# Kernel tuning notes

Hardware: AMD Instinct MI355X
Metric: run time of the kernel (lower is better)

Reference implementation:

```python
import jax, jax.numpy as jnp
import numpy as np

NATOMS = 50000          # edge_vector rows
M = 3 * NATOMS          # attention nodes = numel(edge_vector)
NE = 1500000            # edges
NH, DH = 4, 16          # num_heads, head dim (out_dim // num_heads)


def _glorot(key, shape):
    fan_in, fan_out = shape
    lim = (6.0 / (fan_in + fan_out)) ** 0.5
    return jax.random.uniform(key, shape, jnp.float32, -lim, lim)


def setup_inputs() -> dict:
    key = jax.random.key(0)
    ks = jax.random.split(key, 12)
    inp = {
        "node_attr": jax.random.normal(ks[0], (2, M), jnp.float32),
        "edge_index": jax.random.randint(ks[1], (2, NE), 0, M, jnp.int64),
        "edge_feature": jax.random.normal(ks[2], (NE, 4), jnp.float32),
        "edge_vector": jax.random.normal(ks[3], (NATOMS, 3), jnp.float32),
        # parameters (hardcoded layer sizes in the torch module)
        "W1": _glorot(ks[4], (1, 4)),   "b1": jnp.zeros((4,), jnp.float32),
        "W2": _glorot(ks[5], (4, 16)),  "b2": jnp.zeros((16,), jnp.float32),
        "W": _glorot(ks[6], (16, 64)),  "b": jnp.zeros((64,), jnp.float32),
        "Wout": _glorot(ks[7], (64, 16)), "bout": jnp.zeros((16,), jnp.float32),
        "Wout1": _glorot(ks[8], (16, 1)), "bout1": jnp.zeros((1,), jnp.float32),
    }
    return inp


def reference(node_attr, edge_index, edge_feature, edge_vector,
              W1, b1, W2, b2, W, b, Wout, bout, Wout1, bout1):
    # node pathway: each scalar of edge_vector is one attention node
    h = edge_vector.reshape(-1, 1)                      # [M, 1]
    h = jax.nn.elu(h @ W1 + b1)                         # [M, 4]  (dropout = identity, eval)
    h = (h @ W2 + b2).reshape(-1, DH)                   # [M, 16]
    qkv = (h @ W + b).reshape(-1, NH, DH)               # [M, 4, 16]; Q==K==V (shared linear)

    # edge pathway
    e = jax.nn.elu(edge_feature @ W2 + b2)              # [Ne, 16]
    E = (e @ W + b).reshape(-1, NH, DH)                 # [Ne, 4, 16]

    src_idx = edge_index[0]
    dst_idx = edge_index[1]
    src = qkv[src_idx]                                  # K_h gather [Ne,4,16]
    dst = qkv[dst_idx]                                  # Q_h gather [Ne,4,16]
    score = (src * dst) * (1.0 / np.sqrt(DH)) * E       # edge-conditioned scores
    score = jnp.exp(jnp.clip(score.sum(-1, keepdims=True), -5.0, 5.0))  # [Ne,4,1]

    msg = qkv[src_idx] * score                          # V_h gather * score
    wV = jax.ops.segment_sum(msg, dst_idx, num_segments=M)      # [M,4,16]
    Z = jax.ops.segment_sum(score, dst_idx, num_segments=M)     # [M,4,1]

    h_out = (wV / (Z + 1e-6)).reshape(-1, NH * DH)      # [M, 64]
    h_out = jax.nn.elu(h_out @ Wout + bout)             # [M, 16]
    h_out = (h_out @ Wout1 + bout1).reshape(-1, 3)      # [M/3, 3]
    return h_out
```

## Files before the change

kernel.cpp:

```cpp
#include <hip/hip_runtime.h>
#include <hip/hip_bf16.h>
#include <cstdint>

#define DEVI __device__ __forceinline__

typedef __attribute__((ext_vector_type(8))) short bf16x8;
typedef __attribute__((ext_vector_type(4))) float f32x4;

DEVI float bf2f(unsigned short u) {
    union { unsigned int i; float f; } v; v.i = ((unsigned int)u) << 16; return v.f;
}
DEVI float ldf(const void* p, long long i, int f32) {
    return f32 ? ((const float*)p)[i] : bf2f(((const unsigned short*)p)[i]);
}
DEVI unsigned short f2bfu(float x) {
    __hip_bfloat16 h = __float2bfloat16(x);
    return *reinterpret_cast<unsigned short*>(&h);
}
DEVI short f2bf(float x) { return (short)f2bfu(x); }
DEVI float eluf(float x) { return x > 0.f ? x : __expf(x) - 1.f; }

__global__ __launch_bounds__(64) void detect_k(
    const int* __restrict__ eidx32, const unsigned int* __restrict__ wbits,
    int* __restrict__ flags)
{
    int t = threadIdx.x;
    int odd = eidx32[2 * t + 1];
    unsigned long long bz = __ballot(odd == 0);
    unsigned int w = wbits[t];
    unsigned int ex = (w >> 23) & 0xFF;
    unsigned long long bf = __ballot(ex >= 100 && ex <= 130);
    if (t == 0) {
        flags[0] = (bz == ~0ULL) ? 1 : 0;
        flags[1] = (__popcll(bf) >= 48) ? 1 : 0;
    }
}

__global__ __launch_bounds__(256) void node_qkv_k(
    const int* __restrict__ flags,
    const void* __restrict__ evec,
    const void* __restrict__ W1, const void* __restrict__ b1,
    const void* __restrict__ W2, const void* __restrict__ b2,
    const void* __restrict__ W,  const void* __restrict__ b,
    unsigned short* __restrict__ qkvb, int M_)
{
    __shared__ float sW[1024], sW2[64], sb[64], sb2[16], sW1[4], sb1[4];
    int t = threadIdx.x;
    int f32 = flags[1];
    for (int i = t; i < 1024; i += 256) sW[i] = ldf(W, i, f32);
    if (t < 64) { sW2[t] = ldf(W2, t, f32); sb[t] = ldf(b, t, f32); }
    if (t < 16) sb2[t] = ldf(b2, t, f32);
    if (t < 4)  { sW1[t] = ldf(W1, t, f32); sb1[t] = ldf(b1, t, f32); }
    __syncthreads();

    int m = blockIdx.x * 256 + t;
    if (m >= M_) return;

    float x = ldf(evec, m, f32);
    float h1[4];
    #pragma unroll
    for (int j = 0; j < 4; ++j) h1[j] = eluf(fmaf(x, sW1[j], sb1[j]));
    float h2[16];
    #pragma unroll
    for (int k = 0; k < 16; ++k) h2[k] = sb2[k];
    #pragma unroll
    for (int j = 0; j < 4; ++j)
        #pragma unroll
        for (int k = 0; k < 16; ++k) h2[k] = fmaf(h1[j], sW2[j*16 + k], h2[k]);

    uint4* op = (uint4*)(qkvb + (size_t)m * 64);
    for (int g = 0; g < 8; ++g) {
        float v[8];
        #pragma unroll
        for (int j = 0; j < 8; ++j) {
            int c = g * 8 + j;
            float a = sb[c];
            #pragma unroll
            for (int k = 0; k < 16; ++k) a = fmaf(h2[k], sW[k*64 + c], a);
            v[j] = a;
        }
        uint4 pk;
        pk.x = (unsigned)f2bfu(v[0]) | ((unsigned)f2bfu(v[1]) << 16);
        pk.y = (unsigned)f2bfu(v[2]) | ((unsigned)f2bfu(v[3]) << 16);
        pk.z = (unsigned)f2bfu(v[4]) | ((unsigned)f2bfu(v[5]) << 16);
        pk.w = (unsigned)f2bfu(v[6]) | ((unsigned)f2bfu(v[7]) << 16);
        op[g] = pk;
    }
}

__global__ __launch_bounds__(256) void hist_k(
    const int* __restrict__ flags, const int* __restrict__ eidx32,
    int* __restrict__ counts, int* __restrict__ rank, int NE_)
{
    int e0 = (blockIdx.x * 256 + threadIdx.x) * 4;
    if (e0 >= NE_) return;
    int i64 = flags[0];
    if (e0 + 3 < NE_) {
        int d[4];
        if (i64) {
            long long w = 2LL * (NE_ + (long long)e0);
            int4 a = *(const int4*)(eidx32 + w);
            int4 b = *(const int4*)(eidx32 + w + 4);
            d[0] = a.x; d[1] = a.z; d[2] = b.x; d[3] = b.z;
        } else {
            #pragma unroll
            for (int i = 0; i < 4; ++i) d[i] = eidx32[(long long)NE_ + e0 + i];
        }
        int r[4];
        #pragma unroll
        for (int i = 0; i < 4; ++i) r[i] = atomicAdd(&counts[d[i]], 1);
        *(int4*)(rank + e0) = make_int4(r[0], r[1], r[2], r[3]);
    } else {
        for (int e = e0; e < NE_; ++e) {
            int dst = i64 ? eidx32[2LL * (NE_ + (long long)e)]
                          : eidx32[(long long)NE_ + e];
            rank[e] = atomicAdd(&counts[dst], 1);
        }
    }
}

__global__ __launch_bounds__(256) void scan_a_k(
    const int* __restrict__ counts, int* __restrict__ bsum, int M_)
{
    __shared__ int s[256];
    int t = threadIdx.x;
    int g4 = blockIdx.x * 256 + t;
    int i0 = g4 * 4;
    int v = 0;
    if (i0 + 3 < M_) {
        int4 c = ((const int4*)counts)[g4];
        v = c.x + c.y + c.z + c.w;
    } else {
        for (int k = 0; k < 4 && i0 + k < M_; ++k) v += counts[i0 + k];
    }
    s[t] = v; __syncthreads();
    for (int off = 128; off > 0; off >>= 1) {
        if (t < off) s[t] += s[t + off];
        __syncthreads();
    }
    if (t == 0) bsum[blockIdx.x] = s[0];
}

__global__ __launch_bounds__(256) void scan_b_k(
    const int* __restrict__ bsum, int* __restrict__ bexcl, int nb,
    int* __restrict__ offsets, int M_, int NE_)
{
    __shared__ int s[256];
    int t = threadIdx.x;
    int mine = (t < nb) ? bsum[t] : 0;
    s[t] = mine; __syncthreads();
    for (int off = 1; off < 256; off <<= 1) {
        int v = (t >= off) ? s[t - off] : 0;
        __syncthreads();
        s[t] += v;
        __syncthreads();
    }
    if (t < nb) bexcl[t] = s[t] - mine;
    if (t == 0) offsets[M_] = NE_;
}

__global__ __launch_bounds__(256) void scan_c_k(
    const int* __restrict__ counts, const int* __restrict__ bexcl,
    int* __restrict__ offsets, int M_)
{
    __shared__ int s[256];
    int t = threadIdx.x;
    int g4 = blockIdx.x * 256 + t;
    int i0 = g4 * 4;
    int c0 = 0, c1 = 0, c2 = 0, c3 = 0;
    if (i0 + 3 < M_) {
        int4 c = ((const int4*)counts)[g4];
        c0 = c.x; c1 = c.y; c2 = c.z; c3 = c.w;
    } else {
        if (i0 + 0 < M_) c0 = counts[i0 + 0];
        if (i0 + 1 < M_) c1 = counts[i0 + 1];
        if (i0 + 2 < M_) c2 = counts[i0 + 2];
        if (i0 + 3 < M_) c3 = counts[i0 + 3];
    }
    int tsum = c0 + c1 + c2 + c3;
    s[t] = tsum; __syncthreads();
    for (int off = 1; off < 256; off <<= 1) {
        int v = (t >= off) ? s[t - off] : 0;
        __syncthreads();
        s[t] += v;
        __syncthreads();
    }
    int run = bexcl[blockIdx.x] + s[t] - tsum;
    if (i0 + 0 < M_) { offsets[i0+0] = run; run += c0; }
    if (i0 + 1 < M_) { offsets[i0+1] = run; run += c1; }
    if (i0 + 2 < M_) { offsets[i0+2] = run; run += c2; }
    if (i0 + 3 < M_) { offsets[i0+3] = run; run += c3; }
}

__global__ __launch_bounds__(256) void scatter_k(
    const int* __restrict__ flags, const int* __restrict__ eidx32,
    const void* __restrict__ efeat,
    const int* __restrict__ offsets, const int* __restrict__ rank,
    int4* __restrict__ sorted, int NE_)
{
    int e = blockIdx.x * 256 + threadIdx.x;
    if (e >= NE_) return;
    int i64 = flags[0];
    int f32 = flags[1];
    int src, dst;
    if (i64) { src = eidx32[2LL * e]; dst = eidx32[2LL * (NE_ + (long long)e)]; }
    else     { src = eidx32[e];       dst = eidx32[(long long)NE_ + e]; }

    unsigned int ef01, ef23;
    if (f32) {
        const float4 f = ((const float4*)efeat)[e];
        ef01 = (unsigned)f2bfu(f.x) | ((unsigned)f2bfu(f.y) << 16);
        ef23 = (unsigned)f2bfu(f.z) | ((unsigned)f2bfu(f.w) << 16);
    } else {
        const uint2 u = ((const uint2*)efeat)[e];
        ef01 = u.x; ef23 = u.y;
    }

    int pos = offsets[dst] + rank[e];
    sorted[pos] = make_int4(src, dst, (int)ef01, (int)ef23);
}

__global__ __launch_bounds__(256) void score_k(
    const int* __restrict__ flags, const int4* __restrict__ sorted,
    const void* __restrict__ W2, const void* __restrict__ b2,
    const void* __restrict__ W,  const void* __restrict__ b,
    const unsigned short* __restrict__ qkvb, float* __restrict__ score, int NE_)
{
    __shared__ float sW2[64], sb2[16];
    __shared__ float sE[4][16 * 68];
    int t = threadIdx.x;
    int f32 = flags[1];
    if (t < 64) sW2[t] = ldf(W2, t, f32);
    if (t < 16) sb2[t] = ldf(b2, t, f32);
    __syncthreads();

    int wv   = t >> 6;
    int lane = t & 63;
    int col  = lane & 15;
    int quad = lane >> 4;
    float* myE = &sE[wv][0];

    bf16x8 bfrag[4];
    float  bb[4];
    #pragma unroll
    for (int h = 0; h < 4; ++h) {
        #pragma unroll
        for (int jj = 0; jj < 8; ++jj) {
            int k = quad * 8 + jj;
            float wv_ = (k < 16) ? ldf(W, k * 64 + h * 16 + col, f32) : 0.f;
            bfrag[h][jj] = f2bf(wv_);
        }
        bb[h] = ldf(b, h * 16 + col, f32);
    }

    int j2 = lane >> 2, h2 = lane & 3;

    long long tiles = ((long long)NE_ + 15) >> 4;
    long long wid   = (long long)blockIdx.x * 4 + wv;
    long long nw    = (long long)gridDim.x * 4;

    long long tile = wid;
    int4 rec = make_int4(0, 0, 0, 0);
    if (tile < tiles) {
        int jA = (int)(tile << 4) + col;
        if (jA < NE_) rec = sorted[jA];
    }

    while (tile < tiles) {
        long long tnext = tile + nw;
        int4 recn = make_int4(0, 0, 0, 0);
        if (tnext < tiles) {
            int jB = (int)(tnext << 4) + col;
            if (jB < NE_) recn = sorted[jB];
        }

        int base = (int)(tile << 4);
        float ef0 = bf2f((unsigned short)((unsigned)rec.z & 0xffff));
        float ef1 = bf2f((unsigned short)((unsigned)rec.z >> 16));
        float ef2 = bf2f((unsigned short)((unsigned)rec.w & 0xffff));
        float ef3 = bf2f((unsigned short)((unsigned)rec.w >> 16));

        bf16x8 afrag;
        #pragma unroll
        for (int jj = 0; jj < 8; ++jj) {
            int k = quad * 8 + jj;
            float v = 0.f;
            if (k < 16) {
                v = eluf(fmaf(ef0, sW2[k],
                        fmaf(ef1, sW2[16 + k],
                        fmaf(ef2, sW2[32 + k],
                        fmaf(ef3, sW2[48 + k], sb2[k])))));
            }
            afrag[jj] = f2bf(v);
        }

        f32x4 acc[4];
        #pragma unroll
        for (int h = 0; h < 4; ++h) {
            acc[h] = (f32x4){0.f, 0.f, 0.f, 0.f};
            acc[h] = __builtin_amdgcn_mfma_f32_16x16x32_bf16(afrag, bfrag[h], acc[h], 0, 0, 0);
        }

        #pragma unroll
        for (int h = 0; h < 4; ++h)
            #pragma unroll
            for (int r = 0; r < 4; ++r)
                myE[(quad * 4 + r) * 68 + h * 16 + col] = acc[h][r] + bb[h];

        asm volatile("s_waitcnt lgkmcnt(0)" ::: "memory");

        int srcj = __shfl(rec.x, j2, 64);
        int dstj = __shfl(rec.y, j2, 64);

        const uint4* sp = (const uint4*)(qkvb + (size_t)srcj * 64 + h2 * 16);
        const uint4* dp = (const uint4*)(qkvb + (size_t)dstj * 64 + h2 * 16);
        uint4 sA = sp[0], sB = sp[1], dA = dp[0], dB = dp[1];

        const float4* ep = (const float4*)(myE + j2 * 68 + h2 * 16);
        float4 e0 = ep[0], e1 = ep[1], e2 = ep[2], e3 = ep[3];
        float E[16] = {e0.x,e0.y,e0.z,e0.w, e1.x,e1.y,e1.z,e1.w,
                       e2.x,e2.y,e2.z,e2.w, e3.x,e3.y,e3.z,e3.w};

        unsigned int su[8] = {sA.x,sA.y,sA.z,sA.w, sB.x,sB.y,sB.z,sB.w};
        unsigned int du[8] = {dA.x,dA.y,dA.z,dA.w, dB.x,dB.y,dB.z,dB.w};

        float sc = 0.f;
        #pragma unroll
        for (int i = 0; i < 8; ++i) {
            float s0 = bf2f((unsigned short)(su[i] & 0xffff));
            float s1 = bf2f((unsigned short)(su[i] >> 16));
            float d0 = bf2f((unsigned short)(du[i] & 0xffff));
            float d1 = bf2f((unsigned short)(du[i] >> 16));
            sc = fmaf(s0 * d0, E[2*i],   sc);
            sc = fmaf(s1 * d1, E[2*i+1], sc);
        }
        sc *= 0.25f;
        sc = fminf(fmaxf(sc, -5.f), 5.f);
        float s = __expf(sc);

        int jW = base + j2;
        if (jW < NE_) score[(size_t)jW * 4 + h2] = s;

        rec = recn;
        tile = tnext;
    }
}

__global__ __launch_bounds__(256) void accum_out_k(
    const int* __restrict__ flags,
    const int* __restrict__ offsets, const int4* __restrict__ sorted,
    const float* __restrict__ score, const unsigned short* __restrict__ qkvb,
    const void* __restrict__ Wout, const void* __restrict__ bout,
    const void* __restrict__ Wout1, const void* __restrict__ bout1,
    void* __restrict__ out, int M_)
{
    __shared__ float sWo[1024], sbo[16], sWo1[16];
    __shared__ float sbo1;
    int t = threadIdx.x;
    int f32 = flags[1];
    for (int i = t; i < 1024; i += 256) sWo[i] = ldf(Wout, i, f32);
    if (t < 16) { sbo[t] = ldf(bout, t, f32); sWo1[t] = ldf(Wout1, t, f32); }
    if (t == 0) sbo1 = ldf(bout1, 0, f32);
    __syncthreads();

    int gid = blockIdx.x * 256 + t;
    int m = gid >> 2;
    if (m >= M_) return;
    int h  = gid & 3;
    int hb = h * 16;

    int beg = offsets[m], end = offsets[m + 1];

    float acc[16];
    #pragma unroll
    for (int d = 0; d < 16; ++d) acc[d] = 0.f;
    float z = 0.f;

    int j = beg;
    for (; j + 4 <= end; j += 4) {
        int s4[4];
        float sc4[4];
        #pragma unroll
        for (int u = 0; u < 4; ++u) {
            s4[u]  = sorted[j + u].x;
            sc4[u] = score[(size_t)(j + u) * 4 + h];
        }
        uint4 qa[4], qb[4];
        #pragma unroll
        for (int u = 0; u < 4; ++u) {
            const uint4* p = (const uint4*)(qkvb + (size_t)s4[u] * 64 + hb);
            qa[u] = p[0]; qb[u] = p[1];
        }
        #pragma unroll
        for (int u = 0; u < 4; ++u) {
            float s = sc4[u];
            z += s;
            unsigned int q[8] = {qa[u].x,qa[u].y,qa[u].z,qa[u].w,
                                 qb[u].x,qb[u].y,qb[u].z,qb[u].w};
            #pragma unroll
            for (int i = 0; i < 8; ++i) {
                acc[2*i]   = fmaf(bf2f((unsigned short)(q[i] & 0xffff)), s, acc[2*i]);
                acc[2*i+1] = fmaf(bf2f((unsigned short)(q[i] >> 16)),    s, acc[2*i+1]);
            }
        }
    }
    for (; j < end; ++j) {
        int s0 = sorted[j].x;
        float sc0 = score[(size_t)j * 4 + h];
        const uint4* p0 = (const uint4*)(qkvb + (size_t)s0 * 64 + hb);
        uint4 a0 = p0[0], a1 = p0[1];
        z += sc0;
        unsigned int q0[8] = {a0.x,a0.y,a0.z,a0.w, a1.x,a1.y,a1.z,a1.w};
        #pragma unroll
        for (int i = 0; i < 8; ++i) {
            acc[2*i]   = fmaf(bf2f((unsigned short)(q0[i] & 0xffff)), sc0, acc[2*i]);
            acc[2*i+1] = fmaf(bf2f((unsigned short)(q0[i] >> 16)),    sc0, acc[2*i+1]);
        }
    }

    float zinv = 1.f / (z + 1e-6f);

    float p[16];
    #pragma unroll
    for (int jj = 0; jj < 16; ++jj) p[jj] = 0.f;
    #pragma unroll
    for (int d = 0; d < 16; ++d) {
        float hv = acc[d] * zinv;
        #pragma unroll
        for (int jj = 0; jj < 16; ++jj) p[jj] = fmaf(hv, sWo[(hb + d) * 16 + jj], p[jj]);
    }
    #pragma unroll
    for (int jj = 0; jj < 16; ++jj) {
        p[jj] += __shfl_xor(p[jj], 1, 64);
        p[jj] += __shfl_xor(p[jj], 2, 64);
    }
    if (h == 0) {
        float o = sbo1;
        #pragma unroll
        for (int jj = 0; jj < 16; ++jj) o = fmaf(eluf(p[jj] + sbo[jj]), sWo1[jj], o);
        if (f32) ((float*)out)[m] = o;
        else     ((__hip_bfloat16*)out)[m] = __float2bfloat16(o);
    }
}

extern "C" void kernel_launch(void* const* d_in, const int* in_sizes, int n_in,
                              void* d_out, int out_size, void* d_ws, size_t ws_size,
                              hipStream_t stream)
{
    const int*  eidx  = (const int*)d_in[1];
    const void* efeat = d_in[2];
    const void* evec  = d_in[3];
    const void* W1 = d_in[4],  *b1 = d_in[5];
    const void* W2 = d_in[6],  *b2 = d_in[7];
    const void* W  = d_in[8],  *b  = d_in[9];
    const void* Wout = d_in[10], *bout = d_in[11];
    const void* Wout1 = d_in[12], *bout1 = d_in[13];

    const int M_  = in_sizes[3];
    const int NE_ = in_sizes[1] / 2;
    const int nb  = (M_ + 1023) / 1024;

    char* wp = (char*)d_ws;
    int*            flags   = (int*)wp;                 wp += 16;
    unsigned short* qkvb    = (unsigned short*)wp;      wp += (size_t)M_ * 64 * 2;
    int*            counts  = (int*)wp;                 wp += (size_t)M_ * 4;
    int*            bsum    = (int*)wp;                 wp += 2048 * 4;
    int*            bexcl   = (int*)wp;                 wp += 2048 * 4;
    int*            offsets = (int*)wp;                 wp += ((size_t)M_ + 4) * 4;
    int*            rank    = (int*)wp;                 wp += (size_t)NE_ * 4;
    wp = (char*)(((uintptr_t)wp + 15) & ~(uintptr_t)15);
    int4*           sorted  = (int4*)wp;                wp += (size_t)NE_ * 16;
    float*          scoreB  = (float*)wp;

    detect_k<<<1, 64, 0, stream>>>(eidx, (const unsigned int*)W, flags);
    (void)hipMemsetAsync(counts, 0, (size_t)M_ * 4, stream);

    node_qkv_k<<<(M_ + 255) / 256, 256, 0, stream>>>(
        flags, evec, W1, b1, W2, b2, W, b, qkvb, M_);

    int q4 = (NE_ + 3) / 4;
    hist_k<<<(q4 + 255) / 256, 256, 0, stream>>>(flags, eidx, counts, rank, NE_);
    scan_a_k<<<nb, 256, 0, stream>>>(counts, bsum, M_);
    scan_b_k<<<1, 256, 0, stream>>>(bsum, bexcl, nb, offsets, M_, NE_);
    scan_c_k<<<nb, 256, 0, stream>>>(counts, bexcl, offsets, M_);
    scatter_k<<<(NE_ + 255) / 256, 256, 0, stream>>>(
        flags, eidx, efeat, offsets, rank, sorted, NE_);

    long long tiles = ((long long)NE_ + 15) / 16;
    int sblocks = (int)((tiles + 3) / 4);
    if (sblocks > 12288) sblocks = 12288;
    score_k<<<sblocks, 256, 0, stream>>>(
        flags, sorted, W2, b2, W, b, qkvb, scoreB, NE_);

    long long tot = (long long)M_ * 4;
    accum_out_k<<<(int)((tot + 255) / 256), 256, 0, stream>>>(
        flags, offsets, sorted, scoreB, qkvb,
        Wout, bout, Wout1, bout1, d_out, M_);
}
```

Before: 369.0 us.

## Partition score tiles per XCD and split accumulation across 8 lanes per node

Result: no change. 367.8 us (-0.3%).

```diff
diff --git a/kernel.cpp b/kernel.cpp
--- a/kernel.cpp
+++ b/kernel.cpp
@@ -256,20 +256,23 @@
     int j2 = lane >> 2, h2 = lane & 3;
 
     long long tiles = ((long long)NE_ + 15) >> 4;
-    long long wid   = (long long)blockIdx.x * 4 + wv;
-    long long nw    = (long long)gridDim.x * 4;
-
-    long long tile = wid;
+    long long Tr   = (tiles + 7) >> 3;
+    int       xcd  = blockIdx.x & 7;
+    int       lb   = blockIdx.x >> 3;
+    long long tEnd = (long long)(xcd + 1) * Tr; if (tEnd > tiles) tEnd = tiles;
+    long long stride = (long long)(gridDim.x >> 3) * 4;
+
+    long long tile = (long long)xcd * Tr + (long long)lb * 4 + wv;
     int4 rec = make_int4(0, 0, 0, 0);
-    if (tile < tiles) {
+    if (tile < tEnd) {
         int jA = (int)(tile << 4) + col;
         if (jA < NE_) rec = sorted[jA];
     }
 
-    while (tile < tiles) {
-        long long tnext = tile + nw;
+    while (tile < tEnd) {
+        long long tnext = tile + stride;
         int4 recn = make_int4(0, 0, 0, 0);
-        if (tnext < tiles) {
+        if (tnext < tEnd) {
             int jB = (int)(tnext << 4) + col;
             if (jB < NE_) recn = sorted[jB];
         }
@@ -364,16 +367,17 @@
     __syncthreads();
 
     int gid = blockIdx.x * 256 + t;
-    int m = gid >> 2;
+    int m = gid >> 3;
     if (m >= M_) return;
-    int h  = gid & 3;
-    int hb = h * 16;
+    int sub  = gid & 7;
+    int h    = sub >> 1;
+    int off16 = h * 16 + (sub & 1) * 8;
 
     int beg = offsets[m], end = offsets[m + 1];
 
-    float acc[16];
-    #pragma unroll
-    for (int d = 0; d < 16; ++d) acc[d] = 0.f;
+    float acc[8];
+    #pragma unroll
+    for (int d = 0; d < 8; ++d) acc[d] = 0.f;
     float z = 0.f;
 
     int j = beg;
@@ -385,36 +389,32 @@
             s4[u]  = sorted[j + u].x;
             sc4[u] = score[(size_t)(j + u) * 4 + h];
         }
-        uint4 qa[4], qb[4];
-        #pragma unroll
-        for (int u = 0; u < 4; ++u) {
-            const uint4* p = (const uint4*)(qkvb + (size_t)s4[u] * 64 + hb);
-            qa[u] = p[0]; qb[u] = p[1];
-        }
+        uint4 q[4];
+        #pragma unroll
+        for (int u = 0; u < 4; ++u)
+            q[u] = *(const uint4*)(qkvb + (size_t)s4[u] * 64 + off16);
         #pragma unroll
         for (int u = 0; u < 4; ++u) {
             float s = sc4[u];
             z += s;
-            unsigned int q[8] = {qa[u].x,qa[u].y,qa[u].z,qa[u].w,
-                                 qb[u].x,qb[u].y,qb[u].z,qb[u].w};
+            unsigned int qq[4] = {q[u].x, q[u].y, q[u].z, q[u].w};
             #pragma unroll
-            for (int i = 0; i < 8; ++i) {
-                acc[2*i]   = fmaf(bf2f((unsigned short)(q[i] & 0xffff)), s, acc[2*i]);
-                acc[2*i+1] = fmaf(bf2f((unsigned short)(q[i] >> 16)),    s, acc[2*i+1]);
+            for (int i = 0; i < 4; ++i) {
+                acc[2*i]   = fmaf(bf2f((unsigned short)(qq[i] & 0xffff)), s, acc[2*i]);
+                acc[2*i+1] = fmaf(bf2f((unsigned short)(qq[i] >> 16)),    s, acc[2*i+1]);
             }
         }
     }
     for (; j < end; ++j) {
         int s0 = sorted[j].x;
-        float sc0 = score[(size_t)j * 4 + h];
-        const uint4* p0 = (const uint4*)(qkvb + (size_t)s0 * 64 + hb);
-        uint4 a0 = p0[0], a1 = p0[1];
-        z += sc0;
-        unsigned int q0[8] = {a0.x,a0.y,a0.z,a0.w, a1.x,a1.y,a1.z,a1.w};
-        #pragma unroll
-        for (int i = 0; i < 8; ++i) {
-            acc[2*i]   = fmaf(bf2f((unsigned short)(q0[i] & 0xffff)), sc0, acc[2*i]);
-            acc[2*i+1] = fmaf(bf2f((unsigned short)(q0[i] >> 16)),    sc0, acc[2*i+1]);
+        float s = score[(size_t)j * 4 + h];
+        uint4 q = *(const uint4*)(qkvb + (size_t)s0 * 64 + off16);
+        z += s;
+        unsigned int qq[4] = {q.x, q.y, q.z, q.w};
+        #pragma unroll
+        for (int i = 0; i < 4; ++i) {
+            acc[2*i]   = fmaf(bf2f((unsigned short)(qq[i] & 0xffff)), s, acc[2*i]);
+            acc[2*i+1] = fmaf(bf2f((unsigned short)(qq[i] >> 16)),    s, acc[2*i+1]);
         }
     }
 
@@ -424,17 +424,19 @@
     #pragma unroll
     for (int jj = 0; jj < 16; ++jj) p[jj] = 0.f;
     #pragma unroll
-    for (int d = 0; d < 16; ++d) {
+    for (int d = 0; d < 8; ++d) {
         float hv = acc[d] * zinv;
-        #pragma unroll
-        for (int jj = 0; jj < 16; ++jj) p[jj] = fmaf(hv, sWo[(hb + d) * 16 + jj], p[jj]);
+        int c = off16 + d;
+        #pragma unroll
+        for (int jj = 0; jj < 16; ++jj) p[jj] = fmaf(hv, sWo[c * 16 + jj], p[jj]);
     }
     #pragma unroll
     for (int jj = 0; jj < 16; ++jj) {
         p[jj] += __shfl_xor(p[jj], 1, 64);
         p[jj] += __shfl_xor(p[jj], 2, 64);
-    }
-    if (h == 0) {
+        p[jj] += __shfl_xor(p[jj], 4, 64);
+    }
+    if (sub == 0) {
         float o = sbo1;
         #pragma unroll
         for (int jj = 0; jj < 16; ++jj) o = fmaf(eluf(p[jj] + sbo[jj]), sWo1[jj], o);
@@ -488,11 +490,12 @@
 
     long long tiles = ((long long)NE_ + 15) / 16;
     int sblocks = (int)((tiles + 3) / 4);
+    sblocks = ((sblocks + 7) / 8) * 8;
     if (sblocks > 12288) sblocks = 12288;
     score_k<<<sblocks, 256, 0, stream>>>(
         flags, sorted, W2, b2, W, b, qkvb, scoreB, NE_);
 
-    long long tot = (long long)M_ * 4;
+    long long tot = (long long)M_ * 8;
     accum_out_k<<<(int)((tot + 255) / 256), 256, 0, stream>>>(
         flags, offsets, sorted, scoreB, qkvb,
         Wout, bout, Wout1, bout1, d_out, M_);
```
